# Kernel optimization log

Measured on AMD Instinct MI355X. Metric: run time of the kernel, lower is better.

The kernel has to match this reference:

```python
import jax, jax.numpy as jnp
import numpy as np

B = 64
N_TOTAL = 131072
C_ENC = 128   # base_channels * 4
CTX = 128     # context_dim
HID = 512     # hidden_dim
YDIM = 3
TDIM = 64
HEADS = 4


def timestep_embedding(t, dim=TDIM):
    half = dim // 2
    freqs = jnp.exp(-jnp.arange(half, dtype=jnp.float32) * (np.log(10000.0) / half))
    args = t[:, None].astype(jnp.float32) * freqs[None, :]
    return jnp.concatenate([jnp.sin(args), jnp.cos(args)], axis=-1)


def setup_inputs() -> dict:
    key = jax.random.key(0)
    ks = jax.random.split(key, 32)
    s = 0.05
    p = lambda k, shape: (jax.random.normal(k, shape, jnp.float32) * s)
    inp = {
        "features": jax.random.normal(ks[0], (N_TOTAL, C_ENC), jnp.float32),
        "batch_idx": jnp.sort(jax.random.randint(ks[1], (N_TOTAL,), 0, B)),
        "y_t": jax.random.normal(ks[2], (B, YDIM), jnp.float32),
        "t": jax.random.randint(ks[3], (B,), 0, 1000),
        "N_max": 3328,
        # token_pool
        "Wtok": p(ks[4], (C_ENC, CTX)), "btok": jnp.zeros((CTX,)),
        # time_mlp
        "Wt": p(ks[5], (TDIM, HID)), "bt": jnp.zeros((HID,)),
        # input_proj
        "Win": p(ks[6], (YDIM, HID)), "bin_": jnp.zeros((HID,)),
        # cross-attn pre-projections
        "Wq": p(ks[7], (HID, CTX)), "bq": jnp.zeros((CTX,)),
        "Wk": p(ks[8], (CTX, CTX)), "bk": jnp.zeros((CTX,)),
        "Wv": p(ks[9], (CTX, CTX)), "bv": jnp.zeros((CTX,)),
        # nn.MultiheadAttention in_proj (q,k,v) and out_proj
        "Wiq": p(ks[10], (CTX, CTX)), "biq": jnp.zeros((CTX,)),
        "Wik": p(ks[11], (CTX, CTX)), "bik": jnp.zeros((CTX,)),
        "Wiv": p(ks[12], (CTX, CTX)), "biv": jnp.zeros((CTX,)),
        "Wo": p(ks[13], (CTX, CTX)), "bo": jnp.zeros((CTX,)),
        # cross-attn out: context_dim -> hidden_dim
        "Wco": p(ks[14], (CTX, HID)), "bco": jnp.zeros((HID,)),
        # final output: hidden -> y_dim
        "Wout": p(ks[15], (HID, YDIM)), "bout": jnp.zeros((YDIM,)),
    }
    return inp


def reference(features, batch_idx, y_t, t, N_max,
              Wtok, btok, Wt, bt, Win, bin_, Wq, bq, Wk, bk, Wv, bv,
              Wiq, biq, Wik, bik, Wiv, biv, Wo, bo, Wco, bco, Wout, bout):
    Bsz = y_t.shape[0]
    N = features.shape[0]
    dh = CTX // HEADS

    # encoder token_pool
    feat = features @ Wtok + btok                                      # [N, CTX]

    # fused to_dense_batch: scatter by (batch, within-batch position)
    counts = jax.ops.segment_sum(jnp.ones((N,), jnp.int32), batch_idx,
                                 num_segments=Bsz)                      # [B]
    starts = jnp.cumsum(counts) - counts                                # exclusive cumsum
    pos = jnp.arange(N, dtype=jnp.int32) - starts[batch_idx]            # [N]
    context = jnp.zeros((Bsz, N_max, CTX), feat.dtype).at[batch_idx, pos].set(feat)
    pad_mask = jnp.arange(N_max)[None, :] >= counts[:, None]            # True = padding

    # diffusion head
    t_h = jax.nn.relu(timestep_embedding(t) @ Wt + bt)                  # [B, HID]
    y = y_t @ Win + bin_ + t_h                                          # [B, HID]

    # cross-attention: query=y (1 token), keys/values=context tokens
    q0 = (y @ Wq + bq)                                                  # [B, CTX]
    k0 = context @ Wk + bk                                              # [B, Nm, CTX]
    v0 = context @ Wv + bv
    # MultiheadAttention internal projections
    q = (q0 @ Wiq + biq).reshape(Bsz, HEADS, dh)                        # [B, H, dh]
    k = (k0 @ Wik + bik).reshape(Bsz, N_max, HEADS, dh)
    v = (v0 @ Wiv + biv).reshape(Bsz, N_max, HEADS, dh)
    scores = jnp.einsum('bhd,bnhd->bhn', q, k) / np.sqrt(dh)            # [B, H, Nm]
    scores = jnp.where(pad_mask[:, None, :], -1e9, scores)
    attn = jax.nn.softmax(scores, axis=-1)
    ctx_out = jnp.einsum('bhn,bnhd->bhd', attn, v).reshape(Bsz, CTX)
    attn_out = ctx_out @ Wo + bo                                        # [B, CTX]

    y2 = attn_out @ Wco + bco                                           # [B, HID]
    return y2 @ Wout + bout                                             # [B, YDIM]
```

## Files before the change

kernel.cpp:

```cpp
#include <hip/hip_runtime.h>
#include <hip/hip_bf16.h>


typedef unsigned short ushort_t;
typedef unsigned int uint_t;
typedef unsigned long long ull_t;

#define NB 64
#define CENC 128
#define HID 512
#define RSQRT32 0.17677669529663689f

__device__ __forceinline__ float blo(uint_t u){ return __uint_as_float(u << 16); }
__device__ __forceinline__ float bhi(uint_t u){ return __uint_as_float(u & 0xffff0000u); }
__device__ __forceinline__ float bf2f(ushort_t h){ return __uint_as_float(((uint_t)h) << 16); }
__device__ __forceinline__ ushort_t f2bf(float f){
    uint_t u = __float_as_uint(f);
    u += 0x7fffu + ((u >> 16) & 1u);
    return (ushort_t)(u >> 16);
}

template<bool BF16> struct Ld;
template<> struct Ld<true> {
    static __device__ __forceinline__ float at(const void* p, long i) {
        return __uint_as_float(((uint_t)((const ushort_t*)p)[i]) << 16);
    }
};
template<> struct Ld<false> {
    static __device__ __forceinline__ float at(const void* p, long i) {
        return ((const float*)p)[i];
    }
};

template<bool BF16>
__device__ void kPre_impl(
    const void* Wtok, const void* btok,
    const void* Wk, const void* bk, const void* Wik, const void* bik,
    const void* Wv, const void* bv, const void* Wiv, const void* biv,
    float* UAt, float* VA, float* cv, float* dv, float* tmp)
{
    using L = Ld<BF16>;
    int blk = blockIdx.x, tid = threadIdx.x;
    if (blk < 128) {
        int cx = blk;
        float a = 0.f;
        for (int k = 0; k < 128; k++) a += L::at(Wtok, cx*128+k) * L::at(Wk, k*128+tid);
        tmp[tid] = a; __syncthreads();
        float o = 0.f;
        for (int k = 0; k < 128; k++) o += tmp[k] * L::at(Wik, k*128+tid);
        UAt[tid*128 + cx] = o;
    } else if (blk < 256) {
        int cx = blk - 128;
        float a = 0.f;
        for (int k = 0; k < 128; k++) a += L::at(Wtok, cx*128+k) * L::at(Wv, k*128+tid);
        tmp[tid] = a; __syncthreads();
        float o = 0.f;
        for (int k = 0; k < 128; k++) o += tmp[k] * L::at(Wiv, k*128+tid);
        VA[cx*128 + tid] = o;
    } else if (blk == 256) {
        float a = L::at(bk, tid);
        for (int k = 0; k < 128; k++) a += L::at(btok, k) * L::at(Wk, k*128+tid);
        tmp[tid] = a; __syncthreads();
        float o = L::at(bik, tid);
        for (int k = 0; k < 128; k++) o += tmp[k] * L::at(Wik, k*128+tid);
        cv[tid] = o;
    } else {
        float a = L::at(bv, tid);
        for (int k = 0; k < 128; k++) a += L::at(btok, k) * L::at(Wv, k*128+tid);
        tmp[tid] = a; __syncthreads();
        float o = L::at(biv, tid);
        for (int k = 0; k < 128; k++) o += tmp[k] * L::at(Wiv, k*128+tid);
        dv[tid] = o;
    }
}

__global__ __launch_bounds__(128) void kPre(
    const ushort_t* __restrict__ fraw,
    const void* Wtok, const void* btok,
    const void* Wk, const void* bk, const void* Wik, const void* bik,
    const void* Wv, const void* bv, const void* Wiv, const void* biv,
    int* flag_out, float* UAt, float* VA, float* cv, float* dv)
{
    __shared__ int sbad, szc;
    __shared__ float tmp[128];
    int tid = threadIdx.x;
    if (tid == 0) { sbad = 0; szc = 0; }
    __syncthreads();
    int myb = 0, myz = 0;
    for (int i = tid; i < 4096; i += 128) {
        ushort_t v = fraw[i];
        if (((v >> 7) & 0xff) >= 140) myb = 1;
        if (!(i & 1) && v == 0) myz++;
    }
    if (myb) atomicOr(&sbad, 1);
    atomicAdd(&szc, myz);
    __syncthreads();
    int flag = (sbad || szc > 1024) ? 0 : 1;
    if (blockIdx.x == 0 && tid == 0) *flag_out = flag;
    if (flag) kPre_impl<true >(Wtok,btok,Wk,bk,Wik,bik,Wv,bv,Wiv,biv,UAt,VA,cv,dv,tmp);
    else      kPre_impl<false>(Wtok,btok,Wk,bk,Wik,bik,Wv,bv,Wiv,biv,UAt,VA,cv,dv,tmp);
}

template<bool BF16>
__device__ void kA_impl(
    const void* y_t, const int* t,
    const void* Wt, const void* bt, const void* Win, const void* bin_,
    const void* Wq, const void* bq, const void* Wiq, const void* biq,
    const float* UAt, const float* cv,
    float* u_out, float* cq_out, float* wz, float* lz, float* sh)
{
    using L = Ld<BF16>;
    float* emb = sh;
    float* y   = sh + 64;
    float* p2  = sh + 576;
    float* q0  = sh + 832;
    float* qL  = sh + 960;
    int b = blockIdx.x, tid = threadIdx.x;
    int tid2 = tid & 127, half = tid >> 7;

    for (int i = tid; i < 512; i += 256) wz[b*512 + i] = 0.f;
    if (tid < 4) lz[b*4 + tid] = 0.f;

    if (tid < 32) {
        float fr = __expf(-(float)tid * 0.28782313662425576f);
        float arg = (float)t[b] * fr;
        emb[tid]      = sinf(arg);
        emb[tid + 32] = cosf(arg);
    }
    __syncthreads();

    float yt0 = L::at(y_t, b*3+0), yt1 = L::at(y_t, b*3+1), yt2 = L::at(y_t, b*3+2);
    for (int rep = 0; rep < 2; rep++) {
        int o = tid + rep*256;
        float acc = L::at(bt, o);
        for (int k = 0; k < 64; k++) acc += emb[k] * L::at(Wt, k*512+o);
        acc = fmaxf(acc, 0.f);
        y[o] = acc + L::at(bin_, o) + yt0*L::at(Win, o) + yt1*L::at(Win, 512+o)
             + yt2*L::at(Win, 1024+o);
    }
    __syncthreads();
    {
        float acc = 0.f;
        for (int k = half*256; k < half*256+256; k++) acc += y[k] * L::at(Wq, k*128+tid2);
        p2[half*128 + tid2] = acc;
    }
    __syncthreads();
    if (tid < 128) q0[tid] = p2[tid] + p2[128+tid] + L::at(bq, tid);
    __syncthreads();
    {
        float acc = 0.f;
        for (int k = half*64; k < half*64+64; k++) acc += q0[k] * L::at(Wiq, k*128+tid2);
        p2[half*128 + tid2] = acc;
    }
    __syncthreads();
    if (tid < 128) qL[tid] = p2[tid] + p2[128+tid] + L::at(biq, tid);
    __syncthreads();
    for (int h = half*2; h < half*2+2; h++) {
        float acc = 0.f;
        for (int j = 0; j < 32; j++) acc += UAt[(h*32+j)*128 + tid2] * qL[h*32+j];
        u_out[b*512 + h*128 + tid2] = acc * RSQRT32;
    }
    if (tid < 4) {
        float acc = 0.f;
        for (int j = 0; j < 32; j++) acc += cv[tid*32+j] * qL[tid*32+j];
        cq_out[b*4 + tid] = acc * RSQRT32;
    }
}

__global__ __launch_bounds__(256) void kA(
    const int* __restrict__ flag,
    const void* y_t, const int* t,
    const void* Wt, const void* bt, const void* Win, const void* bin_,
    const void* Wq, const void* bq, const void* Wiq, const void* biq,
    const float* UAt, const float* cv,
    float* u_out, float* cq_out, float* wz, float* lz)
{
    __shared__ float sh[1088];
    if (*flag) kA_impl<true >(y_t,t,Wt,bt,Win,bin_,Wq,bq,Wiq,biq,UAt,cv,u_out,cq_out,wz,lz,sh);
    else       kA_impl<false>(y_t,t,Wt,bt,Win,bin_,Wq,bq,Wiq,biq,UAt,cv,u_out,cq_out,wz,lz,sh);
}

struct alignas(16) KFS {
    ushort_t tile[128*136];
    float eL[128*4];
    int lb[128];
    int starts[65];
    ull_t smask[2];
    int nseg;
};

__global__ __launch_bounds__(256, 4) void kF(
    const int* __restrict__ flag_p,
    const void* __restrict__ features, const int* __restrict__ batch_idx,
    const float* __restrict__ u, const float* __restrict__ cq,
    float* __restrict__ w, float* __restrict__ l)
{
    extern __shared__ char smemraw[];
    KFS* S = (KFS*)smemraw;
    const int base = blockIdx.x * 128;
    const int tau = threadIdx.x;

    if (*flag_p) {
        const ushort_t* src = (const ushort_t*)features + (size_t)base * 128;
        #pragma unroll
        for (int s = 0; s < 8; s++) {
            int idx = s * 256 + tau;
            int ui = idx * 8;
            int tok = ui >> 7, ch = ui & 127;
            uint4 v = ((const uint4*)src)[idx];
            *(uint4*)&S->tile[tok*136 + ch] = v;
        }
    } else {
        const float* src = (const float*)features + (size_t)base * 128;
        #pragma unroll
        for (int s = 0; s < 16; s++) {
            int idx = s * 256 + tau;
            int fi = idx * 4;
            int tok = fi >> 7, ch = fi & 127;
            float4 v = ((const float4*)src)[idx];
            uint_t lo = (uint_t)f2bf(v.x) | ((uint_t)f2bf(v.y) << 16);
            uint_t hi = (uint_t)f2bf(v.z) | ((uint_t)f2bf(v.w) << 16);
            *(uint2*)&S->tile[tok*136 + ch] = make_uint2(lo, hi);
        }
    }
    if (tau < 128) S->lb[tau] = batch_idx[base + tau];
    __syncthreads();

    bool isstart = (tau < 128) && (tau == 0 || S->lb[tau] != S->lb[tau-1]);
    ull_t m = __ballot(isstart);
    int wv = tau >> 6, lane = tau & 63;
    if (wv < 2 && lane == 0) S->smask[wv] = m;
    __syncthreads();
    if (isstart) {
        int rank = ((wv == 1) ? __popcll(S->smask[0]) : 0)
                 + __popcll(m & ((1ull << lane) - 1ull));
        S->starts[rank] = tau;
    }
    if (tau == 0) S->nseg = __popcll(S->smask[0]) + __popcll(S->smask[1]);
    __syncthreads();

    const int qq = tau & 15, grp = tau >> 4;
    const int c = tau & 127, sg = tau >> 7;
    const int nseg = S->nseg;

    for (int s = 0; s < nseg; s++) {
        const int lo = S->starts[s];
        const int hi = (s + 1 < nseg) ? S->starts[s+1] : 128;
        const int b = S->lb[lo];

        const float* ub = u + b*512 + qq*8;
        float4 u0a = *(const float4*)(ub + 0),   u0b = *(const float4*)(ub + 4);
        float4 u1a = *(const float4*)(ub + 128), u1b = *(const float4*)(ub + 132);
        float4 u2a = *(const float4*)(ub + 256), u2b = *(const float4*)(ub + 260);
        float4 u3a = *(const float4*)(ub + 384), u3b = *(const float4*)(ub + 388);
        float4 cqr = *(const float4*)(cq + b*4);

        float l0=0.f, l1=0.f, l2=0.f, l3=0.f;
        for (int tok = lo + grp; tok < hi; tok += 16) {
            uint4 fv = *(const uint4*)&S->tile[tok*136 + qq*8];
            float f0=blo(fv.x), f1=bhi(fv.x), f2=blo(fv.y), f3=bhi(fv.y);
            float f4=blo(fv.z), f5=bhi(fv.z), f6=blo(fv.w), f7=bhi(fv.w);
            float p0 = f0*u0a.x+f1*u0a.y+f2*u0a.z+f3*u0a.w+f4*u0b.x+f5*u0b.y+f6*u0b.z+f7*u0b.w;
            float p1 = f0*u1a.x+f1*u1a.y+f2*u1a.z+f3*u1a.w+f4*u1b.x+f5*u1b.y+f6*u1b.z+f7*u1b.w;
            float p2 = f0*u2a.x+f1*u2a.y+f2*u2a.z+f3*u2a.w+f4*u2b.x+f5*u2b.y+f6*u2b.z+f7*u2b.w;
            float p3 = f0*u3a.x+f1*u3a.y+f2*u3a.z+f3*u3a.w+f4*u3b.x+f5*u3b.y+f6*u3b.z+f7*u3b.w;
            #pragma unroll
            for (int mm = 1; mm < 16; mm <<= 1) {
                p0 += __shfl_xor(p0, mm, 16);
                p1 += __shfl_xor(p1, mm, 16);
                p2 += __shfl_xor(p2, mm, 16);
                p3 += __shfl_xor(p3, mm, 16);
            }
            if (qq == 0) {
                float e0 = __expf(fminf(p0 + cqr.x, 30.f));
                float e1 = __expf(fminf(p1 + cqr.y, 30.f));
                float e2 = __expf(fminf(p2 + cqr.z, 30.f));
                float e3 = __expf(fminf(p3 + cqr.w, 30.f));
                *(float4*)&S->eL[tok*4] = make_float4(e0, e1, e2, e3);
                l0 += e0; l1 += e1; l2 += e2; l3 += e3;
            }
        }
        if (qq == 0) {
            atomicAdd(&l[b*4+0], l0); atomicAdd(&l[b*4+1], l1);
            atomicAdd(&l[b*4+2], l2); atomicAdd(&l[b*4+3], l3);
        }
        __syncthreads();

        float a0=0.f, a1=0.f, a2=0.f, a3=0.f;
        for (int tok = lo + sg; tok < hi; tok += 2) {
            float fvv = bf2f(S->tile[tok*136 + c]);
            float4 e = *(const float4*)&S->eL[tok*4];
            a0 += e.x*fvv; a1 += e.y*fvv; a2 += e.z*fvv; a3 += e.w*fvv;
        }
        atomicAdd(&w[b*512 +   0 + c], a0);
        atomicAdd(&w[b*512 + 128 + c], a1);
        atomicAdd(&w[b*512 + 256 + c], a2);
        atomicAdd(&w[b*512 + 384 + c], a3);
    }
}

template<bool BF16>
__device__ void kE_impl(
    const float* w, const float* l, const float* VA, const float* dv,
    const void* Wo, const void* bo, const void* Wco, const void* bco,
    const void* Wout, const void* bout, void* out, float* sh)
{
    using L = Ld<BF16>;
    float* wb  = sh;
    float* p2  = sh + 512;
    float* ctx = sh + 768;
    float* ao  = sh + 896;
    float* y2  = sh + 1024;
    float* red = sh + 1536;
    int b = blockIdx.x, tid = threadIdx.x;
    int tid2 = tid & 127, half = tid >> 7;

    for (int i = tid; i < 512; i += 256) {
        float lv = l[b*4 + (i >> 7)];
        float inv = (lv > 1e-30f) ? 1.f/lv : 0.f;
        wb[i] = w[b*512 + i] * inv;
    }
    __syncthreads();
    {
        int h = tid2 >> 5;
        float acc = 0.f;
        for (int k = half*64; k < half*64+64; k++) acc += wb[h*128 + k] * VA[k*128 + tid2];
        p2[half*128 + tid2] = acc;
    }
    __syncthreads();
    if (tid < 128) ctx[tid] = p2[tid] + p2[128+tid] + dv[tid];
    __syncthreads();
    {
        float acc = 0.f;
        for (int k = half*64; k < half*64+64; k++) acc += ctx[k] * L::at(Wo, k*128+tid2);
        p2[half*128 + tid2] = acc;
    }
    __syncthreads();
    if (tid < 128) ao[tid] = p2[tid] + p2[128+tid] + L::at(bo, tid);
    __syncthreads();
    for (int rep = 0; rep < 2; rep++) {
        int o = tid + rep*256;
        float acc = L::at(bco, o);
        for (int k = 0; k < 128; k++) acc += ao[k] * L::at(Wco, k*512+o);
        y2[o] = acc;
    }
    __syncthreads();
    for (int o = 0; o < 3; o++) {
        float p = y2[tid]*L::at(Wout, tid*3+o) + y2[tid+256]*L::at(Wout, (tid+256)*3+o);
        red[tid] = p; __syncthreads();
        for (int st = 128; st > 0; st >>= 1) { if (tid < st) red[tid] += red[tid+st]; __syncthreads(); }
        if (tid == 0) {
            float val = red[0] + L::at(bout, o);
            if (BF16) ((ushort_t*)out)[b*3+o] = f2bf(val);
            else      ((float*)out)[b*3+o] = val;
        }
        __syncthreads();
    }
}

__global__ __launch_bounds__(256) void kE(
    const int* __restrict__ flag,
    const float* w, const float* l, const float* VA, const float* dv,
    const void* Wo, const void* bo, const void* Wco, const void* bco,
    const void* Wout, const void* bout, void* out)
{
    __shared__ float sh[1792];
    if (*flag) kE_impl<true >(w,l,VA,dv,Wo,bo,Wco,bco,Wout,bout,out,sh);
    else       kE_impl<false>(w,l,VA,dv,Wo,bo,Wco,bco,Wout,bout,out,sh);
}

extern "C" void kernel_launch(void* const* d_in, const int* in_sizes, int n_in,
                              void* d_out, int out_size, void* d_ws, size_t ws_size,
                              hipStream_t stream)
{
    const void* features = d_in[0];
    const int*  batch_idx= (const int*)d_in[1];
    const void* y_t      = d_in[2];
    const int*  t        = (const int*)d_in[3];
    const void *Wtok=d_in[5],  *btok=d_in[6];
    const void *Wt  =d_in[7],  *bt  =d_in[8];
    const void *Win =d_in[9],  *bin_=d_in[10];
    const void *Wq  =d_in[11], *bq  =d_in[12];
    const void *Wk  =d_in[13], *bk  =d_in[14];
    const void *Wv  =d_in[15], *bv  =d_in[16];
    const void *Wiq =d_in[17], *biq =d_in[18];
    const void *Wik =d_in[19], *bik =d_in[20];
    const void *Wiv =d_in[21], *biv =d_in[22];
    const void *Wo  =d_in[23], *bo  =d_in[24];
    const void *Wco =d_in[25], *bco =d_in[26];
    const void *Wout=d_in[27], *bout=d_in[28];

    int N = in_sizes[0] / CENC;

    float* ws = (float*)d_ws;
    int*   flag = (int*)ws;
    float* u   = ws + 64;
    float* cqv = ws + 64 + 32768;
    float* l   = ws + 64 + 33024;
    float* w   = ws + 64 + 33280;
    float* UAt = ws + 64 + 66048;
    float* VA  = ws + 64 + 82432;
    float* cv  = ws + 64 + 98816;
    float* dv  = ws + 64 + 98944;

    kPre<<<258, 128, 0, stream>>>((const ushort_t*)features,
        Wtok, btok, Wk, bk, Wik, bik, Wv, bv, Wiv, biv, flag, UAt, VA, cv, dv);
    kA<<<NB, 256, 0, stream>>>(flag, y_t, t, Wt, bt, Win, bin_, Wq, bq, Wiq, biq,
        UAt, cv, u, cqv, w, l);
    kF<<<N / 128, 256, sizeof(KFS), stream>>>(flag, features, batch_idx, u, cqv, w, l);
    kE<<<NB, 256, 0, stream>>>(flag, w, l, VA, dv, Wo, bo, Wco, bco, Wout, bout, d_out);
}
```

Measured before the change: 221.8 us.

## Drop weight-precompute kernel and replace global atomics with per-block partial slots

Removes the kPre kernel that precomputed fused Wtok·Wk·Wik and Wtok·Wv·Wiv matrices. Per batch, kA now projects the query back through Wik, Wk and Wtok, and kE applies Wtok, Wv and Wiv to the pooled weighted features. kF stores per-block partial softmax sums and bf16 weighted-feature partials into slots tagged with a header. kE gathers those slots by scanning the headers, and only blocks with more than two segments fall back to atomics. This saves a launch and atomic contention, but adds sequential per-head matvecs in kA and kE, a 2048-entry header scan per batch, and bf16 rounding of the partials.

```diff
diff --git a/kernel.cpp b/kernel.cpp
--- a/kernel.cpp
+++ b/kernel.cpp
@@ -10,6 +10,15 @@
 #define CENC 128
 #define HID 512
 #define RSQRT32 0.17677669529663689f
+
+#define WS_FLAG   0
+#define WS_U      64
+#define WS_CQ     32832
+#define WS_LOVF   33088
+#define WS_WOVF   33344
+#define WS_HDR    66112
+#define WS_LPART  68160
+#define WS_WPART  76352
 
 __device__ __forceinline__ float blo(uint_t u){ return __uint_as_float(u << 16); }
 __device__ __forceinline__ float bhi(uint_t u){ return __uint_as_float(u & 0xffff0000u); }
@@ -32,82 +41,29 @@
     }
 };
 
-template<bool BF16>
-__device__ void kPre_impl(
-    const void* Wtok, const void* btok,
-    const void* Wk, const void* bk, const void* Wik, const void* bik,
-    const void* Wv, const void* bv, const void* Wiv, const void* biv,
-    float* UAt, float* VA, float* cv, float* dv, float* tmp)
-{
-    using L = Ld<BF16>;
-    int blk = blockIdx.x, tid = threadIdx.x;
-    if (blk < 128) {
-        int cx = blk;
-        float a = 0.f;
-        for (int k = 0; k < 128; k++) a += L::at(Wtok, cx*128+k) * L::at(Wk, k*128+tid);
-        tmp[tid] = a; __syncthreads();
-        float o = 0.f;
-        for (int k = 0; k < 128; k++) o += tmp[k] * L::at(Wik, k*128+tid);
-        UAt[tid*128 + cx] = o;
-    } else if (blk < 256) {
-        int cx = blk - 128;
-        float a = 0.f;
-        for (int k = 0; k < 128; k++) a += L::at(Wtok, cx*128+k) * L::at(Wv, k*128+tid);
-        tmp[tid] = a; __syncthreads();
-        float o = 0.f;
-        for (int k = 0; k < 128; k++) o += tmp[k] * L::at(Wiv, k*128+tid);
-        VA[cx*128 + tid] = o;
-    } else if (blk == 256) {
-        float a = L::at(bk, tid);
-        for (int k = 0; k < 128; k++) a += L::at(btok, k) * L::at(Wk, k*128+tid);
-        tmp[tid] = a; __syncthreads();
-        float o = L::at(bik, tid);
-        for (int k = 0; k < 128; k++) o += tmp[k] * L::at(Wik, k*128+tid);
-        cv[tid] = o;
-    } else {
-        float a = L::at(bv, tid);
-        for (int k = 0; k < 128; k++) a += L::at(btok, k) * L::at(Wv, k*128+tid);
-        tmp[tid] = a; __syncthreads();
-        float o = L::at(biv, tid);
-        for (int k = 0; k < 128; k++) o += tmp[k] * L::at(Wiv, k*128+tid);
-        dv[tid] = o;
-    }
-}
-
-__global__ __launch_bounds__(128) void kPre(
-    const ushort_t* __restrict__ fraw,
-    const void* Wtok, const void* btok,
-    const void* Wk, const void* bk, const void* Wik, const void* bik,
-    const void* Wv, const void* bv, const void* Wiv, const void* biv,
-    int* flag_out, float* UAt, float* VA, float* cv, float* dv)
-{
-    __shared__ int sbad, szc;
-    __shared__ float tmp[128];
-    int tid = threadIdx.x;
-    if (tid == 0) { sbad = 0; szc = 0; }
+__device__ int detect_bf16(const ushort_t* f, int tid, int nthr, int* sh2) {
+    if (tid == 0) { sh2[0] = 0; sh2[1] = 0; }
     __syncthreads();
     int myb = 0, myz = 0;
-    for (int i = tid; i < 4096; i += 128) {
-        ushort_t v = fraw[i];
+    for (int i = tid; i < 4096; i += nthr) {
+        ushort_t v = f[i];
         if (((v >> 7) & 0xff) >= 140) myb = 1;
         if (!(i & 1) && v == 0) myz++;
     }
-    if (myb) atomicOr(&sbad, 1);
-    atomicAdd(&szc, myz);
-    __syncthreads();
-    int flag = (sbad || szc > 1024) ? 0 : 1;
-    if (blockIdx.x == 0 && tid == 0) *flag_out = flag;
-    if (flag) kPre_impl<true >(Wtok,btok,Wk,bk,Wik,bik,Wv,bv,Wiv,biv,UAt,VA,cv,dv,tmp);
-    else      kPre_impl<false>(Wtok,btok,Wk,bk,Wik,bik,Wv,bv,Wiv,biv,UAt,VA,cv,dv,tmp);
+    if (myb) atomicOr(&sh2[0], 1);
+    atomicAdd(&sh2[1], myz);
+    __syncthreads();
+    return (sh2[0] || sh2[1] > 1024) ? 0 : 1;
 }
 
 template<bool BF16>
-__device__ void kA_impl(
+__device__ void kA_impl(int b, int tid,
     const void* y_t, const int* t,
     const void* Wt, const void* bt, const void* Win, const void* bin_,
     const void* Wq, const void* bq, const void* Wiq, const void* biq,
-    const float* UAt, const float* cv,
-    float* u_out, float* cq_out, float* wz, float* lz, float* sh)
+    const void* Wtok, const void* btok, const void* Wk, const void* bk,
+    const void* Wik, const void* bik,
+    float* u_out, float* cq_out, float* w_ovf, float* l_ovf, float* sh)
 {
     using L = Ld<BF16>;
     float* emb = sh;
@@ -115,11 +71,13 @@
     float* p2  = sh + 576;
     float* q0  = sh + 832;
     float* qL  = sh + 960;
-    int b = blockIdx.x, tid = threadIdx.x;
+    float* tb  = sh + 1088;
+    float* t1  = sh + 1216;
+    float* t2  = q0;
     int tid2 = tid & 127, half = tid >> 7;
 
-    for (int i = tid; i < 512; i += 256) wz[b*512 + i] = 0.f;
-    if (tid < 4) lz[b*4 + tid] = 0.f;
+    for (int i = tid; i < 512; i += 256) w_ovf[b*512 + i] = 0.f;
+    if (tid < 4) l_ovf[b*4 + tid] = 0.f;
 
     if (tid < 32) {
         float fr = __expf(-(float)tid * 0.28782313662425576f);
@@ -155,52 +113,107 @@
     __syncthreads();
     if (tid < 128) qL[tid] = p2[tid] + p2[128+tid] + L::at(biq, tid);
     __syncthreads();
-    for (int h = half*2; h < half*2+2; h++) {
+    {
         float acc = 0.f;
-        for (int j = 0; j < 32; j++) acc += UAt[(h*32+j)*128 + tid2] * qL[h*32+j];
-        u_out[b*512 + h*128 + tid2] = acc * RSQRT32;
-    }
-    if (tid < 4) {
-        float acc = 0.f;
-        for (int j = 0; j < 32; j++) acc += cv[tid*32+j] * qL[tid*32+j];
-        cq_out[b*4 + tid] = acc * RSQRT32;
+        for (int k = half*64; k < half*64+64; k++)
+            acc += L::at(btok, k) * L::at(Wk, k*128+tid2);
+        p2[half*128 + tid2] = acc;
+    }
+    __syncthreads();
+    if (tid < 128) tb[tid] = p2[tid] + p2[128+tid] + L::at(bk, tid);
+    __syncthreads();
+
+    for (int h = 0; h < 4; h++) {
+        {
+            float a = 0.f;
+            for (int j = half*16; j < half*16+16; j++)
+                a += L::at(Wik, tid2*128 + h*32 + j) * qL[h*32 + j];
+            p2[half*128 + tid2] = a;
+        }
+        __syncthreads();
+        if (tid < 128) t1[tid] = p2[tid] + p2[128+tid];
+        __syncthreads();
+        if (tid < 128) {
+            float r = tb[tid] * t1[tid];
+            if (tid < 32) r += L::at(bik, h*32 + tid) * qL[h*32 + tid];
+            p2[tid] = r;
+        }
+        __syncthreads();
+        for (int s = 64; s > 0; s >>= 1) { if (tid < s) p2[tid] += p2[tid+s]; __syncthreads(); }
+        if (tid == 0) cq_out[b*4 + h] = p2[0] * RSQRT32;
+        __syncthreads();
+        {
+            float a = 0.f;
+            for (int k = half*64; k < half*64+64; k++)
+                a += L::at(Wk, tid2*128 + k) * t1[k];
+            p2[half*128 + tid2] = a;
+        }
+        __syncthreads();
+        if (tid < 128) t2[tid] = p2[tid] + p2[128+tid];
+        __syncthreads();
+        {
+            float a = 0.f;
+            for (int k = half*64; k < half*64+64; k++)
+                a += L::at(Wtok, tid2*128 + k) * t2[k];
+            p2[half*128 + tid2] = a;
+        }
+        __syncthreads();
+        if (tid < 128) u_out[b*512 + h*128 + tid] = (p2[tid] + p2[128+tid]) * RSQRT32;
+        __syncthreads();
     }
 }
 
 __global__ __launch_bounds__(256) void kA(
-    const int* __restrict__ flag,
+    const ushort_t* __restrict__ fraw,
     const void* y_t, const int* t,
     const void* Wt, const void* bt, const void* Win, const void* bin_,
     const void* Wq, const void* bq, const void* Wiq, const void* biq,
-    const float* UAt, const float* cv,
-    float* u_out, float* cq_out, float* wz, float* lz)
+    const void* Wtok, const void* btok, const void* Wk, const void* bk,
+    const void* Wik, const void* bik,
+    float* ws)
 {
-    __shared__ float sh[1088];
-    if (*flag) kA_impl<true >(y_t,t,Wt,bt,Win,bin_,Wq,bq,Wiq,biq,UAt,cv,u_out,cq_out,wz,lz,sh);
-    else       kA_impl<false>(y_t,t,Wt,bt,Win,bin_,Wq,bq,Wiq,biq,UAt,cv,u_out,cq_out,wz,lz,sh);
+    __shared__ int sh2[2];
+    __shared__ float sh[1344];
+    int flag = detect_bf16(fraw, threadIdx.x, 256, sh2);
+    if (blockIdx.x == 0 && threadIdx.x == 0) *(int*)(ws + WS_FLAG) = flag;
+    if (flag) kA_impl<true >(blockIdx.x, threadIdx.x, y_t,t,Wt,bt,Win,bin_,Wq,bq,Wiq,biq,
+                             Wtok,btok,Wk,bk,Wik,bik,
+                             ws+WS_U, ws+WS_CQ, ws+WS_WOVF, ws+WS_LOVF, sh);
+    else      kA_impl<false>(blockIdx.x, threadIdx.x, y_t,t,Wt,bt,Win,bin_,Wq,bq,Wiq,biq,
+                             Wtok,btok,Wk,bk,Wik,bik,
+                             ws+WS_U, ws+WS_CQ, ws+WS_WOVF, ws+WS_LOVF, sh);
 }
 
 struct alignas(16) KFS {
     ushort_t tile[128*136];
     float eL[128*4];
+    float red[16*4];
     int lb[128];
-    int starts[65];
+    int starts[129];
     ull_t smask[2];
     int nseg;
+    int sh2pad[4];
 };
 
 __global__ __launch_bounds__(256, 4) void kF(
-    const int* __restrict__ flag_p,
     const void* __restrict__ features, const int* __restrict__ batch_idx,
-    const float* __restrict__ u, const float* __restrict__ cq,
-    float* __restrict__ w, float* __restrict__ l)
+    float* __restrict__ ws)
 {
     extern __shared__ char smemraw[];
     KFS* S = (KFS*)smemraw;
     const int base = blockIdx.x * 128;
     const int tau = threadIdx.x;
-
-    if (*flag_p) {
+    const float* u  = ws + WS_U;
+    const float* cq = ws + WS_CQ;
+    float* l_ovf = ws + WS_LOVF;
+    float* w_ovf = ws + WS_WOVF;
+    int*   hdr   = (int*)(ws + WS_HDR);
+    float* lpart = ws + WS_LPART;
+    ushort_t* wpart = (ushort_t*)(ws + WS_WPART);
+
+    const int flag = *(const int*)(ws + WS_FLAG);
+
+    if (flag) {
         const ushort_t* src = (const ushort_t*)features + (size_t)base * 128;
         #pragma unroll
         for (int s = 0; s < 8; s++) {
@@ -239,14 +252,18 @@
     if (tau == 0) S->nseg = __popcll(S->smask[0]) + __popcll(S->smask[1]);
     __syncthreads();
 
+    const int nseg = S->nseg;
+    if (tau < 2) hdr[blockIdx.x*2 + tau] = (tau < nseg) ? S->lb[S->starts[tau]] : -1;
+
     const int qq = tau & 15, grp = tau >> 4;
-    const int c = tau & 127, sg = tau >> 7;
-    const int nseg = S->nseg;
+    const int c = tau & 127, hp = tau >> 7;
 
     for (int s = 0; s < nseg; s++) {
         const int lo = S->starts[s];
         const int hi = (s + 1 < nseg) ? S->starts[s+1] : 128;
         const int b = S->lb[lo];
+        const bool slotpath = (s < 2);
+        const int slot = blockIdx.x*2 + s;
 
         const float* ub = u + b*512 + qq*8;
         float4 u0a = *(const float4*)(ub + 0),   u0b = *(const float4*)(ub + 4);
@@ -280,77 +297,154 @@
                 l0 += e0; l1 += e1; l2 += e2; l3 += e3;
             }
         }
-        if (qq == 0) {
-            atomicAdd(&l[b*4+0], l0); atomicAdd(&l[b*4+1], l1);
-            atomicAdd(&l[b*4+2], l2); atomicAdd(&l[b*4+3], l3);
-        }
-        __syncthreads();
-
-        float a0=0.f, a1=0.f, a2=0.f, a3=0.f;
-        for (int tok = lo + sg; tok < hi; tok += 2) {
+        if (qq == 0) *(float4*)&S->red[grp*4] = make_float4(l0, l1, l2, l3);
+        __syncthreads();
+
+        if (tau < 4) {
+            float ls = 0.f;
+            #pragma unroll
+            for (int g = 0; g < 16; g++) ls += S->red[g*4 + tau];
+            if (slotpath) lpart[slot*4 + tau] = ls;
+            else atomicAdd(&l_ovf[b*4 + tau], ls);
+        }
+
+        float a0 = 0.f, a1 = 0.f;
+        for (int tok = lo; tok < hi; tok++) {
             float fvv = bf2f(S->tile[tok*136 + c]);
-            float4 e = *(const float4*)&S->eL[tok*4];
-            a0 += e.x*fvv; a1 += e.y*fvv; a2 += e.z*fvv; a3 += e.w*fvv;
-        }
-        atomicAdd(&w[b*512 +   0 + c], a0);
-        atomicAdd(&w[b*512 + 128 + c], a1);
-        atomicAdd(&w[b*512 + 256 + c], a2);
-        atomicAdd(&w[b*512 + 384 + c], a3);
+            float2 e = *(const float2*)&S->eL[tok*4 + 2*hp];
+            a0 += e.x * fvv; a1 += e.y * fvv;
+        }
+        if (slotpath) {
+            wpart[slot*512 + (2*hp)*128 + c]   = f2bf(a0);
+            wpart[slot*512 + (2*hp+1)*128 + c] = f2bf(a1);
+        } else {
+            atomicAdd(&w_ovf[b*512 + (2*hp)*128 + c], a0);
+            atomicAdd(&w_ovf[b*512 + (2*hp+1)*128 + c], a1);
+        }
+        __syncthreads();
     }
 }
 
 template<bool BF16>
-__device__ void kE_impl(
-    const float* w, const float* l, const float* VA, const float* dv,
-    const void* Wo, const void* bo, const void* Wco, const void* bco,
-    const void* Wout, const void* bout, void* out, float* sh)
+__device__ void kE_impl(int b, int tid, float* ws,
+    const void* Wtok, const void* btok, const void* Wv, const void* bv,
+    const void* Wiv, const void* biv, const void* Wo, const void* bo,
+    const void* Wco, const void* bco, const void* Wout, const void* bout,
+    void* out, float* sh, int* shi)
 {
     using L = Ld<BF16>;
     float* wb  = sh;
     float* p2  = sh + 512;
-    float* ctx = sh + 768;
-    float* ao  = sh + 896;
-    float* y2  = sh + 1024;
-    float* red = sh + 1536;
-    int b = blockIdx.x, tid = threadIdx.x;
+    float* s1  = sh + 768;
+    float* s2  = sh + 896;
+    float* ctx = sh + 1024;
+    float* ao  = sh + 1152;
+    float* y2  = sh + 1280;
+    float* linv= sh + 1792;
+    int* mslot = shi;
+    int* manyp = shi + 64;
+
+    const int* hdr = (const int*)(ws + WS_HDR);
+    const float* lpart = ws + WS_LPART;
+    const ushort_t* wpart = (const ushort_t*)(ws + WS_WPART);
+    const float* l_ovf = ws + WS_LOVF;
+    const float* w_ovf = ws + WS_WOVF;
+
     int tid2 = tid & 127, half = tid >> 7;
-
-    for (int i = tid; i < 512; i += 256) {
-        float lv = l[b*4 + (i >> 7)];
-        float inv = (lv > 1e-30f) ? 1.f/lv : 0.f;
-        wb[i] = w[b*512 + i] * inv;
-    }
-    __syncthreads();
+    int ch0 = tid, ch1 = tid + 256;
+    float a0 = 0.f, a1 = 0.f, lacc = 0.f;
+
+    for (int cb = 0; cb < 2048; cb += 64) {
+        if (tid < 64) {
+            int hv = hdr[cb + tid];
+            bool mt = (hv == b);
+            ull_t mk = __ballot(mt);
+            mslot[tid] = mt ? (cb + tid) : -1;
+            if (tid == 0) *manyp = (mk != 0ull) ? 1 : 0;
+        }
+        __syncthreads();
+        if (*manyp) {
+            for (int j = 0; j < 64; j++) {
+                int s = mslot[j];
+                if (s >= 0) {
+                    a0 += bf2f(wpart[s*512 + ch0]);
+                    a1 += bf2f(wpart[s*512 + ch1]);
+                    if (tid < 4) lacc += lpart[s*4 + tid];
+                }
+            }
+        }
+        __syncthreads();
+    }
+    a0 += w_ovf[b*512 + ch0];
+    a1 += w_ovf[b*512 + ch1];
+    if (tid < 4) {
+        lacc += l_ovf[b*4 + tid];
+        linv[tid] = (lacc > 1e-30f) ? 1.f/lacc : 0.f;
+    }
+    __syncthreads();
+    wb[ch0] = a0 * linv[ch0 >> 7];
+    wb[ch1] = a1 * linv[ch1 >> 7];
+    __syncthreads();
+
+    for (int h = 0; h < 4; h++) {
+        {
+            float a = 0.f;
+            for (int k = half*64; k < half*64+64; k++)
+                a += wb[h*128 + k] * L::at(Wtok, k*128 + tid2);
+            p2[half*128 + tid2] = a;
+        }
+        __syncthreads();
+        if (tid < 128) s1[tid] = p2[tid] + p2[128+tid] + L::at(btok, tid);
+        __syncthreads();
+        {
+            float a = 0.f;
+            for (int k = half*64; k < half*64+64; k++)
+                a += s1[k] * L::at(Wv, k*128 + tid2);
+            p2[half*128 + tid2] = a;
+        }
+        __syncthreads();
+        if (tid < 128) s2[tid] = p2[tid] + p2[128+tid] + L::at(bv, tid);
+        __syncthreads();
+        {
+            int d = tid & 31, q8 = tid >> 5;
+            float a = 0.f;
+            for (int k = q8*16; k < q8*16+16; k++)
+                a += s2[k] * L::at(Wiv, k*128 + h*32 + d);
+            p2[q8*32 + d] = a;
+        }
+        __syncthreads();
+        if (tid < 32) {
+            float a = L::at(biv, h*32 + tid);
+            #pragma unroll
+            for (int q = 0; q < 8; q++) a += p2[q*32 + tid];
+            ctx[h*32 + tid] = a;
+        }
+        __syncthreads();
+    }
+
     {
-        int h = tid2 >> 5;
-        float acc = 0.f;
-        for (int k = half*64; k < half*64+64; k++) acc += wb[h*128 + k] * VA[k*128 + tid2];
-        p2[half*128 + tid2] = acc;
-    }
-    __syncthreads();
-    if (tid < 128) ctx[tid] = p2[tid] + p2[128+tid] + dv[tid];
-    __syncthreads();
-    {
-        float acc = 0.f;
-        for (int k = half*64; k < half*64+64; k++) acc += ctx[k] * L::at(Wo, k*128+tid2);
-        p2[half*128 + tid2] = acc;
+        float a = 0.f;
+        for (int k = half*64; k < half*64+64; k++)
+            a += ctx[k] * L::at(Wo, k*128 + tid2);
+        p2[half*128 + tid2] = a;
     }
     __syncthreads();
     if (tid < 128) ao[tid] = p2[tid] + p2[128+tid] + L::at(bo, tid);
     __syncthreads();
     for (int rep = 0; rep < 2; rep++) {
         int o = tid + rep*256;
-        float acc = L::at(bco, o);
-        for (int k = 0; k < 128; k++) acc += ao[k] * L::at(Wco, k*512+o);
-        y2[o] = acc;
+        float a = L::at(bco, o);
+        for (int k = 0; k < 128; k++) a += ao[k] * L::at(Wco, k*512 + o);
+        y2[o] = a;
     }
     __syncthreads();
     for (int o = 0; o < 3; o++) {
         float p = y2[tid]*L::at(Wout, tid*3+o) + y2[tid+256]*L::at(Wout, (tid+256)*3+o);
-        red[tid] = p; __syncthreads();
-        for (int st = 128; st > 0; st >>= 1) { if (tid < st) red[tid] += red[tid+st]; __syncthreads(); }
+        p2[tid] = p;
+        __syncthreads();
+        for (int st = 128; st > 0; st >>= 1) { if (tid < st) p2[tid] += p2[tid+st]; __syncthreads(); }
         if (tid == 0) {
-            float val = red[0] + L::at(bout, o);
+            float val = p2[0] + L::at(bout, o);
             if (BF16) ((ushort_t*)out)[b*3+o] = f2bf(val);
             else      ((float*)out)[b*3+o] = val;
         }
@@ -359,14 +453,19 @@
 }
 
 __global__ __launch_bounds__(256) void kE(
-    const int* __restrict__ flag,
-    const float* w, const float* l, const float* VA, const float* dv,
-    const void* Wo, const void* bo, const void* Wco, const void* bco,
-    const void* Wout, const void* bout, void* out)
+    float* ws,
+    const void* Wtok, const void* btok, const void* Wv, const void* bv,
+    const void* Wiv, const void* biv, const void* Wo, const void* bo,
+    const void* Wco, const void* bco, const void* Wout, const void* bout,
+    void* out)
 {
-    __shared__ float sh[1792];
-    if (*flag) kE_impl<true >(w,l,VA,dv,Wo,bo,Wco,bco,Wout,bout,out,sh);
-    else       kE_impl<false>(w,l,VA,dv,Wo,bo,Wco,bco,Wout,bout,out,sh);
+    __shared__ float sh[1800];
+    __shared__ int shi[66];
+    int flag = *(const int*)(ws + WS_FLAG);
+    if (flag) kE_impl<true >(blockIdx.x, threadIdx.x, ws, Wtok,btok,Wv,bv,Wiv,biv,
+                             Wo,bo,Wco,bco,Wout,bout,out,sh,shi);
+    else      kE_impl<false>(blockIdx.x, threadIdx.x, ws, Wtok,btok,Wv,bv,Wiv,biv,
+                             Wo,bo,Wco,bco,Wout,bout,out,sh,shi);
 }
 
 extern "C" void kernel_launch(void* const* d_in, const int* in_sizes, int n_in,
@@ -391,22 +490,11 @@
     const void *Wout=d_in[27], *bout=d_in[28];
 
     int N = in_sizes[0] / CENC;
-
     float* ws = (float*)d_ws;
-    int*   flag = (int*)ws;
-    float* u   = ws + 64;
-    float* cqv = ws + 64 + 32768;
-    float* l   = ws + 64 + 33024;
-    float* w   = ws + 64 + 33280;
-    float* UAt = ws + 64 + 66048;
-    float* VA  = ws + 64 + 82432;
-    float* cv  = ws + 64 + 98816;
-    float* dv  = ws + 64 + 98944;
-
-    kPre<<<258, 128, 0, stream>>>((const ushort_t*)features,
-        Wtok, btok, Wk, bk, Wik, bik, Wv, bv, Wiv, biv, flag, UAt, VA, cv, dv);
-    kA<<<NB, 256, 0, stream>>>(flag, y_t, t, Wt, bt, Win, bin_, Wq, bq, Wiq, biq,
-        UAt, cv, u, cqv, w, l);
-    kF<<<N / 128, 256, sizeof(KFS), stream>>>(flag, features, batch_idx, u, cqv, w, l);
-    kE<<<NB, 256, 0, stream>>>(flag, w, l, VA, dv, Wo, bo, Wco, bco, Wout, bout, d_out);
-}
+
+    kA<<<NB, 256, 0, stream>>>((const ushort_t*)features, y_t, t,
+        Wt, bt, Win, bin_, Wq, bq, Wiq, biq, Wtok, btok, Wk, bk, Wik, bik, ws);
+    kF<<<N / 128, 256, sizeof(KFS), stream>>>(features, batch_idx, ws);
+    kE<<<NB, 256, 0, stream>>>(ws, Wtok, btok, Wv, bv, Wiv, biv, Wo, bo,
+                               Wco, bco, Wout, bout, d_out);
+}
```

New measurement: 293.8 us. 32.5% more time.
